# Performance work log

Measured on AMD Instinct MI355X. Metric: run time of the kernel, lower is better.

Reference implementation:

```python
import jax, jax.numpy as jnp
from jax import lax
import numpy as np

SIGMAS = (30.0, 150.0, 300.0)
RESTORE_FACTOR = 2.0
COLOR_GAIN = 10.0
GAIN = 270.0
OFFSET = 128.0
EPS = 1e-6


def _dwconv(x, k2d, stride):
    # depthwise 2D conv, NCHW, VALID padding (caller pads)
    C = x.shape[1]
    kh, kw = k2d.shape
    w = jnp.broadcast_to(k2d.astype(x.dtype)[None, None], (C, 1, kh, kw))
    return lax.conv_general_dilated(
        x, w, (stride, stride), 'VALID',
        dimension_numbers=('NCHW', 'OIHW', 'NCHW'),
        feature_group_count=C)


def _pyr_down(x):
    # cv2.pyrDown: 5x5 binomial kernel, reflect-101 border, stride-2 decimation
    k1 = jnp.array([1., 4., 6., 4., 1.], jnp.float32) / 16.0
    k2 = jnp.outer(k1, k1)
    xp = jnp.pad(x, ((0, 0), (0, 0), (2, 2), (2, 2)), mode='reflect')
    return _dwconv(xp, k2, 2)


def _gauss_blur(x, ksize):
    # cv2.GaussianBlur with sigmaX=0: sigma derived from kernel size
    s = 0.3 * ((ksize - 1) * 0.5 - 1.0) + 0.8
    i = jnp.arange(ksize, dtype=jnp.float32) - (ksize - 1) / 2.0
    g = jnp.exp(-(i * i) / (2.0 * s * s))
    g = g / g.sum()
    k2 = jnp.outer(g, g)
    p = ksize // 2
    xp = jnp.pad(x, ((0, 0), (0, 0), (p, p), (p, p)), mode='reflect')
    return _dwconv(xp, k2, 1)


def _fast_filter(x, sigma):
    # Faithful port of GaussianBlurConv.FastFilter (static Python recursion:
    # sigma is a compile-time constant, so depth is fixed at trace time).
    sigma = min(sigma, 300.0)
    k = int(round(sigma * 3 * 2 + 1)) | 1
    if k < 3:
        return x
    if k < 10:
        return _gauss_blur(x, k)
    h, w = x.shape[2], x.shape[3]
    if h < 2 or w < 2:
        return x
    sub = _fast_filter(_pyr_down(x), sigma / 2.0)
    # cv2.resize default INTER_LINEAR == half-pixel bilinear
    return jax.image.resize(sub, (x.shape[0], x.shape[1], h, w), method='bilinear')


def _msr_forward(x):
    img = x * 255.0 + 1.0                      # (N,3,H,W)
    log_img = jnp.log10(img + EPS)
    retinex = sum(log_img - jnp.log10(_fast_filter(img, s) + EPS) for s in SIGMAS)
    retinex = retinex / len(SIGMAS)
    img_sum = jnp.sum(img, axis=1, keepdims=True)   # (N,1,H,W)
    color_rest = jnp.log10(img * RESTORE_FACTOR / (img_sum + EPS) + 1.0)
    enhanced = retinex * color_rest * COLOR_GAIN * GAIN + OFFSET
    return jnp.clip(enhanced, 0.0, 255.0) / 255.0


def setup_inputs() -> dict:
    key = jax.random.key(0)
    x = jax.random.uniform(key, (8, 3, 1280, 1280), dtype=jnp.float32)
    return {"x": x}


def reference(x):
    return _msr_forward(x)
```

## Files before the change

kernel.cpp:

```cpp
#include <hip/hip_runtime.h>

#define NC 24

typedef float f32x4 __attribute__((ext_vector_type(4)));

__device__ __forceinline__ float pyr_point(const float* ip, int Hi, int Wi, int oy, int ox)
{
    const float k1[5] = {0.0625f, 0.25f, 0.375f, 0.25f, 0.0625f};
    float acc = 0.f;
#pragma unroll
    for (int i = 0; i < 5; ++i) {
        int y = 2 * oy - 2 + i;
        y = (y < 0) ? -y : y;
        y = (y >= Hi) ? (2 * Hi - 2 - y) : y;
        const float* rp = ip + (size_t)y * Wi;
        float r = 0.f;
#pragma unroll
        for (int j = 0; j < 5; ++j) {
            int xx = 2 * ox - 2 + j;
            xx = (xx < 0) ? -xx : xx;
            xx = (xx >= Wi) ? (2 * Wi - 2 - xx) : xx;
            r = fmaf(k1[j], rp[xx], r);
        }
        acc = fmaf(k1[i], r, acc);
    }
    return acc;
}

template <int K>
__device__ __forceinline__ float blur_point(const float* ip, int H, int W, int oy, int ox,
                                            const float* w)
{
    const int R = K / 2;
    float acc = 0.f;
#pragma unroll
    for (int i = 0; i < K; ++i) {
        int y = oy - R + i;
        y = (y < 0) ? -y : y;
        y = (y >= H) ? (2 * H - 2 - y) : y;
        const float* rp = ip + (size_t)y * W;
        float r = 0.f;
#pragma unroll
        for (int j = 0; j < K; ++j) {
            int xx = ox - R + j;
            xx = (xx < 0) ? -xx : xx;
            xx = (xx >= W) ? (2 * W - 2 - xx) : xx;
            r = fmaf(w[j], rp[xx], r);
        }
        acc = fmaf(w[i], r, acc);
    }
    return acc;
}

__global__ void __launch_bounds__(256) pyrdown_lds_kernel(
    const float* __restrict__ in, float* __restrict__ out,
    int Hi, int Wi, int Ho, int Wo, float scale, float offs)
{
    const int TW = 132;
    __shared__ float vs[16 * TW];
    const int tid = threadIdx.x;
    const int OX = blockIdx.x * 64;
    const int OY = blockIdx.y * 16;
    const int nc = blockIdx.z;
    const float k1[5] = {0.0625f, 0.25f, 0.375f, 0.25f, 0.0625f};
    const float* ip = in + (size_t)nc * Hi * Wi;

    for (int idx = tid; idx < 16 * TW; idx += 256) {
        int r = idx / TW;
        int c = idx - r * TW;
        int oy = OY + r;
        if (oy >= Ho) oy = Ho - 1;
        int xc = 2 * OX - 2 + c;
        xc = (xc < 0) ? -xc : xc;
        xc = (xc >= Wi) ? (2 * Wi - 2 - xc) : xc;
        xc = max(0, min(Wi - 1, xc));
        float acc = 0.f;
#pragma unroll
        for (int i = 0; i < 5; ++i) {
            int y = 2 * oy - 2 + i;
            y = (y < 0) ? -y : y;
            y = (y >= Hi) ? (2 * Hi - 2 - y) : y;
            acc = fmaf(k1[i], ip[(size_t)y * Wi + xc], acc);
        }
        vs[idx] = acc;
    }
    __syncthreads();

    for (int o = tid; o < 1024; o += 256) {
        int r = o >> 6, c = o & 63;
        int ox = OX + c, oy = OY + r;
        if (ox >= Wo || oy >= Ho) continue;
        const float* vp = &vs[r * TW + 2 * c];
        float s = 0.f;
#pragma unroll
        for (int j = 0; j < 5; ++j) s = fmaf(k1[j], vp[j], s);
        out[((size_t)nc * Ho + oy) * Wo + ox] = fmaf(s, scale, offs);
    }
}

__global__ void __launch_bounds__(256) base_kernel(
    const float* __restrict__ L4g, float* __restrict__ b30g,
    float* __restrict__ b150g, float* __restrict__ b300g)
{
    __shared__ float sL4[80 * 80];
    __shared__ float sL5[40 * 40];
    __shared__ float sL6[20 * 20];
    __shared__ float sL7[10 * 10];
    __shared__ float sL8[5 * 5];
    const int nc = blockIdx.x;
    const int tid = threadIdx.x;

    float w7[7], w9[9];
    {
        float s = 1.4f, s2 = 2.f * s * s, sum = 0.f;
#pragma unroll
        for (int i = 0; i < 7; ++i) { float d = (float)i - 3.f; w7[i] = expf(-(d * d) / s2); sum += w7[i]; }
#pragma unroll
        for (int i = 0; i < 7; ++i) w7[i] /= sum;
        s = 1.7f; s2 = 2.f * s * s; sum = 0.f;
#pragma unroll
        for (int i = 0; i < 9; ++i) { float d = (float)i - 4.f; w9[i] = expf(-(d * d) / s2); sum += w9[i]; }
#pragma unroll
        for (int i = 0; i < 9; ++i) w9[i] /= sum;
    }

    const float* src = L4g + (size_t)nc * 6400;
    for (int i = tid; i < 1600; i += 256)
        *(f32x4*)&sL4[4 * i] = *(const f32x4*)&src[4 * i];
    __syncthreads();
    for (int i = tid; i < 1600; i += 256) {
        int oy = i / 40, ox = i - oy * 40;
        sL5[i] = pyr_point(sL4, 80, 80, oy, ox);
    }
    __syncthreads();
    for (int i = tid; i < 400; i += 256) {
        int oy = i / 20, ox = i - oy * 20;
        sL6[i] = pyr_point(sL5, 40, 40, oy, ox);
    }
    __syncthreads();
    for (int i = tid; i < 100; i += 256) {
        int oy = i / 10, ox = i - oy * 10;
        sL7[i] = pyr_point(sL6, 20, 20, oy, ox);
    }
    __syncthreads();
    for (int i = tid; i < 25; i += 256) {
        int oy = i / 5, ox = i - oy * 5;
        sL8[i] = pyr_point(sL7, 10, 10, oy, ox);
    }
    __syncthreads();
    for (int i = tid; i < 1600; i += 256) {
        int oy = i / 40, ox = i - oy * 40;
        b30g[(size_t)nc * 1600 + i] = blur_point<7>(sL5, 40, 40, oy, ox, w7);
    }
    for (int i = tid; i < 100; i += 256) {
        int oy = i / 10, ox = i - oy * 10;
        b150g[(size_t)nc * 100 + i] = blur_point<9>(sL7, 10, 10, oy, ox, w9);
    }
    for (int i = tid; i < 25; i += 256) {
        int oy = i / 5, ox = i - oy * 5;
        b300g[(size_t)nc * 25 + i] = blur_point<9>(sL8, 5, 5, oy, ox, w9);
    }
}

#define CH 1721
#define O30_3 0
#define O30_2 36
#define O30_1 100
#define O30_0 244
#define O150_5 568
#define O150_4 593
#define O150_3 618
#define O150_2 654
#define O150_1 718
#define O150_0 862
#define O300_6 1186
#define O300_5 1211
#define O300_4 1236
#define O300_3 1261
#define O300_2 1297
#define O300_1 1333
#define O300_0 1397

template <int NPL, int ND, int NS, int LSD>
__device__ __forceinline__ void up_level(float* __restrict__ S,
                                         const int (&srcO)[NPL], const int (&dstO)[NPL],
                                         int ayD, int axD, int ayS, int axS)
{
    const int SSRC = LSD / 2;
    const int NPTS = ND * ND;
    for (int pt = threadIdx.x; pt < NPTS; pt += 256) {
        int ry = pt / ND, rx = pt - ry * ND;
        int gy = min(max(ayD + ry, 0), LSD - 1);
        int gx = min(max(axD + rx, 0), LSD - 1);
        int my = gy >> 1, py = gy & 1;
        int mx = gx >> 1, px = gx & 1;
        int yA = py ? my : max(my - 1, 0);
        int yB = py ? min(my + 1, SSRC - 1) : my;
        float wyA = py ? 0.75f : 0.25f;
        float wyB = 1.0f - wyA;
        int xA = px ? mx : max(mx - 1, 0);
        int xB = px ? min(mx + 1, SSRC - 1) : mx;
        float wxA = px ? 0.75f : 0.25f;
        float wxB = 1.0f - wxA;
        int la = (yA - ayS) * NS + (xA - axS);
        int laB = la + (xB - xA);
        int lb = (yB - ayS) * NS + (xA - axS);
        int lbB = lb + (xB - xA);
#pragma unroll
        for (int p = 0; p < NPL; ++p) {
            const float* sp = S + srcO[p];
            float v = wyA * fmaf(wxA, sp[la], wxB * sp[laB]) +
                      wyB * fmaf(wxA, sp[lb], wxB * sp[lbB]);
            S[dstO[p] + pt] = v;
        }
    }
}

__global__ void __launch_bounds__(256) mega_final(
    const float* __restrict__ x,
    const float* __restrict__ b30g,
    const float* __restrict__ b150g,
    const float* __restrict__ b300g,
    float* __restrict__ out)
{
    const int H = 1280, W = 1280;
    __shared__ float S[3 * CH];

    const int tid = threadIdx.x;
    const int X0 = blockIdx.x * 64, Y0 = blockIdx.y * 64;
    const int n = blockIdx.z;

    int ay[7], ax[7];
    ay[0] = (Y0 >> 2) - 1;
    ax[0] = (X0 >> 2) - 1;
#pragma unroll
    for (int l = 1; l < 7; ++l) {
        ay[l] = (ay[l - 1] >> 1) - 1;
        ax[l] = (ax[l - 1] >> 1) - 1;
    }

    if (tid < 36) {
        int ry = tid / 6, rx = tid - ry * 6;
        int gy = min(max(ay[3] + ry, 0), 39);
        int gx = min(max(ax[3] + rx, 0), 39);
#pragma unroll
        for (int c = 0; c < 3; ++c)
            S[c * CH + O30_3 + tid] = b30g[(size_t)(n * 3 + c) * 1600 + gy * 40 + gx];
    } else if (tid >= 64 && tid < 89) {
        int t = tid - 64;
        int ry = t / 5, rx = t - ry * 5;
        int gy = min(max(ay[5] + ry, 0), 9);
        int gx = min(max(ax[5] + rx, 0), 9);
#pragma unroll
        for (int c = 0; c < 3; ++c)
            S[c * CH + O150_5 + t] = b150g[(size_t)(n * 3 + c) * 100 + gy * 10 + gx];
    } else if (tid >= 128 && tid < 153) {
        int t = tid - 128;
        int ry = t / 5, rx = t - ry * 5;
        int gy = min(max(ay[6] + ry, 0), 4);
        int gx = min(max(ax[6] + rx, 0), 4);
#pragma unroll
        for (int c = 0; c < 3; ++c)
            S[c * CH + O300_6 + t] = b300g[(size_t)(n * 3 + c) * 25 + gy * 5 + gx];
    }
    __syncthreads();

    {
        const int s[3] = {O300_6, O300_6 + CH, O300_6 + 2 * CH};
        const int d[3] = {O300_5, O300_5 + CH, O300_5 + 2 * CH};
        up_level<3, 5, 5, 10>(S, s, d, ay[5], ax[5], ay[6], ax[6]);
    }
    __syncthreads();
    {
        const int s[6] = {O300_5, O300_5 + CH, O300_5 + 2 * CH, O150_5, O150_5 + CH, O150_5 + 2 * CH};
        const int d[6] = {O300_4, O300_4 + CH, O300_4 + 2 * CH, O150_4, O150_4 + CH, O150_4 + 2 * CH};
        up_level<6, 5, 5, 20>(S, s, d, ay[4], ax[4], ay[5], ax[5]);
    }
    __syncthreads();
    {
        const int s[6] = {O300_4, O300_4 + CH, O300_4 + 2 * CH, O150_4, O150_4 + CH, O150_4 + 2 * CH};
        const int d[6] = {O300_3, O300_3 + CH, O300_3 + 2 * CH, O150_3, O150_3 + CH, O150_3 + 2 * CH};
        up_level<6, 6, 5, 40>(S, s, d, ay[3], ax[3], ay[4], ax[4]);
    }
    __syncthreads();
    {
        const int s[9] = {O300_3, O300_3 + CH, O300_3 + 2 * CH, O150_3, O150_3 + CH, O150_3 + 2 * CH,
                          O30_3, O30_3 + CH, O30_3 + 2 * CH};
        const int d[9] = {O300_2, O300_2 + CH, O300_2 + 2 * CH, O150_2, O150_2 + CH, O150_2 + 2 * CH,
                          O30_2, O30_2 + CH, O30_2 + 2 * CH};
        up_level<9, 8, 6, 80>(S, s, d, ay[2], ax[2], ay[3], ax[3]);
    }
    __syncthreads();
    {
        const int s[9] = {O300_2, O300_2 + CH, O300_2 + 2 * CH, O150_2, O150_2 + CH, O150_2 + 2 * CH,
                          O30_2, O30_2 + CH, O30_2 + 2 * CH};
        const int d[9] = {O300_1, O300_1 + CH, O300_1 + 2 * CH, O150_1, O150_1 + CH, O150_1 + 2 * CH,
                          O30_1, O30_1 + CH, O30_1 + 2 * CH};
        up_level<9, 12, 8, 160>(S, s, d, ay[1], ax[1], ay[2], ax[2]);
    }
    __syncthreads();
    {
        const int s[9] = {O300_1, O300_1 + CH, O300_1 + 2 * CH, O150_1, O150_1 + CH, O150_1 + 2 * CH,
                          O30_1, O30_1 + CH, O30_1 + 2 * CH};
        const int d[9] = {O300_0, O300_0 + CH, O300_0 + 2 * CH, O150_0, O150_0 + CH, O150_0 + 2 * CH,
                          O30_0, O30_0 + CH, O30_0 + 2 * CH};
        up_level<9, 18, 12, 320>(S, s, d, ay[0], ax[0], ay[1], ax[1]);
    }
    __syncthreads();

    int tyi = tid >> 4, txi = tid & 15;
    int byi = (Y0 >> 2) + tyi, bxi = (X0 >> 2) + txi;
    int ry[3], rx[3];
    ry[0] = max(byi - 1, 0) - ay[0]; ry[1] = byi - ay[0]; ry[2] = min(byi + 1, 319) - ay[0];
    rx[0] = max(bxi - 1, 0) - ax[0]; rx[1] = bxi - ax[0]; rx[2] = min(bxi + 1, 319) - ax[0];
    const int ol0[3] = {O30_0, O150_0, O300_0};

    f32x4 xi[3][4];
#pragma unroll
    for (int c = 0; c < 3; ++c)
#pragma unroll
        for (int qy = 0; qy < 4; ++qy)
            xi[c][qy] = __builtin_nontemporal_load(
                (const f32x4*)&x[((size_t)(n * 3 + c) * H + 4 * byi + qy) * W + 4 * bxi]);

    float crcp[4][4];
#pragma unroll
    for (int qy = 0; qy < 4; ++qy)
#pragma unroll
        for (int qx = 0; qx < 4; ++qx) {
            float s = (xi[0][qy][qx] + xi[1][qy][qx] + xi[2][qy][qx]) * 255.f + 3.f;
            crcp[qy][qx] = __fdividef(2.f, s + 1e-6f);
        }

#pragma unroll
    for (int c = 0; c < 3; ++c) {
        float prod[4][4];
#pragma unroll
        for (int qy = 0; qy < 4; ++qy)
#pragma unroll
            for (int qx = 0; qx < 4; ++qx) prod[qy][qx] = 1.f;

#pragma unroll
        for (int s = 0; s < 3; ++s) {
            const float* fp = &S[c * CH + ol0[s]];
            float v[3][3];
#pragma unroll
            for (int i = 0; i < 3; ++i)
#pragma unroll
                for (int j = 0; j < 3; ++j) v[i][j] = fp[ry[i] * 18 + rx[j]];
            float cy[4][3];
#pragma unroll
            for (int j = 0; j < 3; ++j) {
                float v0 = v[0][j], v1 = v[1][j], v2 = v[2][j];
                cy[0][j] = fmaf(0.375f, v0, 0.625f * v1);
                cy[1][j] = fmaf(0.1875f, v0, fmaf(0.75f, v1, 0.0625f * v2));
                cy[2][j] = fmaf(0.0625f, v0, fmaf(0.75f, v1, 0.1875f * v2));
                cy[3][j] = fmaf(0.625f, v1, 0.375f * v2);
            }
#pragma unroll
            for (int qy = 0; qy < 4; ++qy) {
                float a0 = cy[qy][0], a1 = cy[qy][1], a2 = cy[qy][2];
                float t0 = fmaf(0.375f, a0, 0.625f * a1);
                float t1 = fmaf(0.1875f, a0, fmaf(0.75f, a1, 0.0625f * a2));
                float t2 = fmaf(0.0625f, a0, fmaf(0.75f, a1, 0.1875f * a2));
                float t3 = fmaf(0.625f, a1, 0.375f * a2);
                prod[qy][0] *= (t0 + 1e-6f);
                prod[qy][1] *= (t1 + 1e-6f);
                prod[qy][2] *= (t2 + 1e-6f);
                prod[qy][3] *= (t3 + 1e-6f);
            }
        }

#pragma unroll
        for (int qy = 0; qy < 4; ++qy) {
            f32x4 o;
#pragma unroll
            for (int qx = 0; qx < 4; ++qx) {
                float img = xi[c][qy][qx] * 255.f + 1.f;
                float a = img + 1e-6f;
                float l2a = __log2f(__fdividef(a * a * a, prod[qy][qx]));
                float carg = fmaf(img, crcp[qy][qx], 1.f);
                float l2c = __log2f(carg);
                float e = fmaf(l2a * l2c, 81.55715246f, 128.f);
                e = fminf(fmaxf(e, 0.f), 255.f);
                o[qx] = e * (1.f / 255.f);
            }
            __builtin_nontemporal_store(
                o, (f32x4*)&out[((size_t)(n * 3 + c) * H + 4 * byi + qy) * W + 4 * bxi]);
        }
    }
}

extern "C" void kernel_launch(void* const* d_in, const int* in_sizes, int n_in,
                              void* d_out, int out_size, void* d_ws, size_t ws_size,
                              hipStream_t stream)
{
    const float* x = (const float*)d_in[0];
    float* out = (float*)d_out;
    float* ws = (float*)d_ws;

    size_t off = 0;
    auto alloc = [&](int d) { float* p = ws + off; off += (size_t)NC * d * d; return p; };
    float* L1 = alloc(640);
    float* L2 = alloc(320);
    float* L3 = alloc(160);
    float* L4 = alloc(80);
    float* b30 = alloc(40);
    float* b150 = alloc(10);
    float* b300 = alloc(5);
    (void)ws_size; (void)in_sizes; (void)n_in; (void)out_size;

    dim3 blk(256, 1, 1);
    auto gridP = [&](int Wo, int Ho) { return dim3((Wo + 63) / 64, (Ho + 15) / 16, NC); };

    pyrdown_lds_kernel<<<gridP(640, 640), blk, 0, stream>>>(x,  L1, 1280, 1280, 640, 640, 255.f, 1.f);
    pyrdown_lds_kernel<<<gridP(320, 320), blk, 0, stream>>>(L1, L2, 640, 640, 320, 320, 1.f, 0.f);
    pyrdown_lds_kernel<<<gridP(160, 160), blk, 0, stream>>>(L2, L3, 320, 320, 160, 160, 1.f, 0.f);
    pyrdown_lds_kernel<<<gridP(80,  80),  blk, 0, stream>>>(L3, L4, 160, 160, 80, 80, 1.f, 0.f);
    base_kernel<<<dim3(NC, 1, 1), dim3(256, 1, 1), 0, stream>>>(L4, b30, b150, b300);
    mega_final<<<dim3(20, 20, 8), dim3(256, 1, 1), 0, stream>>>(x, b30, b150, b300, out);
}
```

Baseline: 356.2 us.

## Fuse L3/L4 pyramid levels into single per-channel tail kernel

Replaces two pyrdown kernel launches and the base kernel with one 1024-thread block per image channel. That block computes L3 from L2 in shared memory in row strips, then L4 and the coarser levels plus the blurs. It removes two launches and the global round trips for L3 and L4. In exchange, only 24 blocks do the 320->160 level, which underuses the GPU, and shared memory use grows to about 140KB per block.

```diff
diff --git a/kernel.cpp b/kernel.cpp
--- a/kernel.cpp
+++ b/kernel.cpp
@@ -98,10 +98,12 @@
     }
 }
 
-__global__ void __launch_bounds__(256) base_kernel(
-    const float* __restrict__ L4g, float* __restrict__ b30g,
+__global__ void __launch_bounds__(1024) fused_tail(
+    const float* __restrict__ L2g, float* __restrict__ b30g,
     float* __restrict__ b150g, float* __restrict__ b300g)
 {
+    __shared__ float sL3[160 * 160];
+    __shared__ float vs[8 * 324];
     __shared__ float sL4[80 * 80];
     __shared__ float sL5[40 * 40];
     __shared__ float sL6[20 * 20];
@@ -109,6 +111,8 @@
     __shared__ float sL8[5 * 5];
     const int nc = blockIdx.x;
     const int tid = threadIdx.x;
+    const float k1[5] = {0.0625f, 0.25f, 0.375f, 0.25f, 0.0625f};
+    const float* ip = L2g + (size_t)nc * 320 * 320;
 
     float w7[7], w9[9];
     {
@@ -124,39 +128,71 @@
         for (int i = 0; i < 9; ++i) w9[i] /= sum;
     }
 
-    const float* src = L4g + (size_t)nc * 6400;
-    for (int i = tid; i < 1600; i += 256)
-        *(f32x4*)&sL4[4 * i] = *(const f32x4*)&src[4 * i];
-    __syncthreads();
-    for (int i = tid; i < 1600; i += 256) {
+    for (int st = 0; st < 20; ++st) {
+        const int OY = st * 8;
+        for (int idx = tid; idx < 8 * 324; idx += 1024) {
+            int r = idx / 324, c = idx - r * 324;
+            int oy = OY + r;
+            int xc = c - 2;
+            xc = (xc < 0) ? -xc : xc;
+            xc = (xc >= 320) ? (638 - xc) : xc;
+            float acc = 0.f;
+#pragma unroll
+            for (int i = 0; i < 5; ++i) {
+                int y = 2 * oy - 2 + i;
+                y = (y < 0) ? -y : y;
+                y = (y >= 320) ? (638 - y) : y;
+                acc = fmaf(k1[i], ip[y * 320 + xc], acc);
+            }
+            vs[idx] = acc;
+        }
+        __syncthreads();
+        for (int o = tid; o < 8 * 160; o += 1024) {
+            int r = o / 160, c = o - r * 160;
+            const float* vp = &vs[r * 324 + 2 * c];
+            float s = 0.f;
+#pragma unroll
+            for (int j = 0; j < 5; ++j) s = fmaf(k1[j], vp[j], s);
+            sL3[(OY + r) * 160 + c] = s;
+        }
+        __syncthreads();
+    }
+
+    for (int i = tid; i < 6400; i += 1024) {
+        int oy = i / 80, ox = i - oy * 80;
+        sL4[i] = pyr_point(sL3, 160, 160, oy, ox);
+    }
+    __syncthreads();
+    for (int i = tid; i < 1600; i += 1024) {
         int oy = i / 40, ox = i - oy * 40;
         sL5[i] = pyr_point(sL4, 80, 80, oy, ox);
     }
     __syncthreads();
-    for (int i = tid; i < 400; i += 256) {
+    for (int i = tid; i < 400; i += 1024) {
         int oy = i / 20, ox = i - oy * 20;
         sL6[i] = pyr_point(sL5, 40, 40, oy, ox);
     }
     __syncthreads();
-    for (int i = tid; i < 100; i += 256) {
+    for (int i = tid; i < 100; i += 1024) {
         int oy = i / 10, ox = i - oy * 10;
         sL7[i] = pyr_point(sL6, 20, 20, oy, ox);
     }
     __syncthreads();
-    for (int i = tid; i < 25; i += 256) {
+    for (int i = tid; i < 25; i += 1024) {
         int oy = i / 5, ox = i - oy * 5;
         sL8[i] = pyr_point(sL7, 10, 10, oy, ox);
     }
     __syncthreads();
-    for (int i = tid; i < 1600; i += 256) {
+
+    for (int i = tid; i < 1600; i += 1024) {
         int oy = i / 40, ox = i - oy * 40;
         b30g[(size_t)nc * 1600 + i] = blur_point<7>(sL5, 40, 40, oy, ox, w7);
     }
-    for (int i = tid; i < 100; i += 256) {
+    for (int i = tid; i < 100; i += 1024) {
         int oy = i / 10, ox = i - oy * 10;
         b150g[(size_t)nc * 100 + i] = blur_point<9>(sL7, 10, 10, oy, ox, w9);
     }
-    for (int i = tid; i < 25; i += 256) {
+    for (int i = tid; i < 25; i += 1024) {
         int oy = i / 5, ox = i - oy * 5;
         b300g[(size_t)nc * 25 + i] = blur_point<9>(sL8, 5, 5, oy, ox, w9);
     }
@@ -403,8 +439,6 @@
     auto alloc = [&](int d) { float* p = ws + off; off += (size_t)NC * d * d; return p; };
     float* L1 = alloc(640);
     float* L2 = alloc(320);
-    float* L3 = alloc(160);
-    float* L4 = alloc(80);
     float* b30 = alloc(40);
     float* b150 = alloc(10);
     float* b300 = alloc(5);
@@ -415,8 +449,6 @@
 
     pyrdown_lds_kernel<<<gridP(640, 640), blk, 0, stream>>>(x,  L1, 1280, 1280, 640, 640, 255.f, 1.f);
     pyrdown_lds_kernel<<<gridP(320, 320), blk, 0, stream>>>(L1, L2, 640, 640, 320, 320, 1.f, 0.f);
-    pyrdown_lds_kernel<<<gridP(160, 160), blk, 0, stream>>>(L2, L3, 320, 320, 160, 160, 1.f, 0.f);
-    pyrdown_lds_kernel<<<gridP(80,  80),  blk, 0, stream>>>(L3, L4, 160, 160, 80, 80, 1.f, 0.f);
-    base_kernel<<<dim3(NC, 1, 1), dim3(256, 1, 1), 0, stream>>>(L4, b30, b150, b300);
+    fused_tail<<<dim3(NC, 1, 1), dim3(1024, 1, 1), 0, stream>>>(L2, b30, b150, b300);
     mega_final<<<dim3(20, 20, 8), dim3(256, 1, 1), 0, stream>>>(x, b30, b150, b300, out);
 }
```

After: 376.4 us. 5.7% more time.

## Fuse pairs of pyrDown levels into one kernel, skipping L1 and L3 buffers

Applied to the files above, without the earlier changes.

Replaces the four separate pyrDown launches with two launches of a kernel that does two consecutive pyrDown levels in shared memory. It computes the intermediate level tile with halo in LDS, so the L1 and L3 global round trips and two launches go away. The base kernel also moves to 512 threads per block. In exchange it recomputes halo rows, uses far more LDS per block (lower occupancy), and the second fused launch has few blocks.

```diff
diff --git a/kernel.cpp b/kernel.cpp
--- a/kernel.cpp
+++ b/kernel.cpp
@@ -52,37 +52,65 @@
     return acc;
 }
 
-__global__ void __launch_bounds__(256) pyrdown_lds_kernel(
+__global__ void __launch_bounds__(256) dpyrdown_kernel(
     const float* __restrict__ in, float* __restrict__ out,
-    int Hi, int Wi, int Ho, int Wo, float scale, float offs)
-{
-    const int TW = 132;
-    __shared__ float vs[16 * TW];
+    int Hi, int Wi, int Hm, int Wm, int Ho, int Wo, float scale, float offs)
+{
+    __shared__ float vsA[35 * 268];
+    __shared__ float l1t[35 * 132];
+    __shared__ float vsC[16 * 132];
     const int tid = threadIdx.x;
     const int OX = blockIdx.x * 64;
     const int OY = blockIdx.y * 16;
     const int nc = blockIdx.z;
     const float k1[5] = {0.0625f, 0.25f, 0.375f, 0.25f, 0.0625f};
     const float* ip = in + (size_t)nc * Hi * Wi;
-
-    for (int idx = tid; idx < 16 * TW; idx += 256) {
-        int r = idx / TW;
-        int c = idx - r * TW;
-        int oy = OY + r;
-        if (oy >= Ho) oy = Ho - 1;
-        int xc = 2 * OX - 2 + c;
-        xc = (xc < 0) ? -xc : xc;
-        xc = (xc >= Wi) ? (2 * Wi - 2 - xc) : xc;
-        xc = max(0, min(Wi - 1, xc));
+    const int baseX = 4 * OX - 6;
+    const int baseY1 = 2 * OY - 2;
+
+    for (int idx = tid; idx < 35 * 268; idx += 256) {
+        int r = idx / 268, c = idx - r * 268;
+        int y1 = baseY1 + r;
+        int xi = baseX + c;
+        xi = (xi < 0) ? -xi : xi;
+        xi = (xi >= Wi) ? (2 * Wi - 2 - xi) : xi;
+        xi = min(max(xi, 0), Wi - 1);
         float acc = 0.f;
 #pragma unroll
         for (int i = 0; i < 5; ++i) {
-            int y = 2 * oy - 2 + i;
+            int y = 2 * y1 - 2 + i;
             y = (y < 0) ? -y : y;
             y = (y >= Hi) ? (2 * Hi - 2 - y) : y;
-            acc = fmaf(k1[i], ip[(size_t)y * Wi + xc], acc);
-        }
-        vs[idx] = acc;
+            y = min(max(y, 0), Hi - 1);
+            acc = fmaf(k1[i], ip[(size_t)y * Wi + xi], acc);
+        }
+        vsA[idx] = acc;
+    }
+    __syncthreads();
+
+    for (int idx = tid; idx < 35 * 132; idx += 256) {
+        int r = idx / 132, lc = idx - r * 132;
+        const float* vp = &vsA[r * 268 + 2 * lc];
+        float acc = 0.f;
+#pragma unroll
+        for (int j = 0; j < 5; ++j) acc = fmaf(k1[j], vp[j], acc);
+        l1t[idx] = acc;
+    }
+    __syncthreads();
+
+    for (int idx = tid; idx < 16 * 132; idx += 256) {
+        int rr = idx / 132, lc = idx - rr * 132;
+        int y1n0 = baseY1 + 2 * rr;
+        float acc = 0.f;
+#pragma unroll
+        for (int i = 0; i < 5; ++i) {
+            int y1 = y1n0 + i;
+            y1 = (y1 < 0) ? -y1 : y1;
+            y1 = (y1 >= Hm) ? (2 * Hm - 2 - y1) : y1;
+            int ly = min(max(y1 - baseY1, 0), 34);
+            acc = fmaf(k1[i], l1t[ly * 132 + lc], acc);
+        }
+        vsC[idx] = acc;
     }
     __syncthreads();
 
@@ -90,15 +118,20 @@
         int r = o >> 6, c = o & 63;
         int ox = OX + c, oy = OY + r;
         if (ox >= Wo || oy >= Ho) continue;
-        const float* vp = &vs[r * TW + 2 * c];
-        float s = 0.f;
-#pragma unroll
-        for (int j = 0; j < 5; ++j) s = fmaf(k1[j], vp[j], s);
-        out[((size_t)nc * Ho + oy) * Wo + ox] = fmaf(s, scale, offs);
-    }
-}
-
-__global__ void __launch_bounds__(256) base_kernel(
+        float acc = 0.f;
+#pragma unroll
+        for (int j = 0; j < 5; ++j) {
+            int c1 = 2 * ox - 2 + j;
+            c1 = (c1 < 0) ? -c1 : c1;
+            c1 = (c1 >= Wm) ? (2 * Wm - 2 - c1) : c1;
+            int lc = min(max(c1 - (2 * OX - 2), 0), 131);
+            acc = fmaf(k1[j], vsC[r * 132 + lc], acc);
+        }
+        out[((size_t)nc * Ho + oy) * Wo + ox] = fmaf(acc, scale, offs);
+    }
+}
+
+__global__ void __launch_bounds__(512) base_kernel(
     const float* __restrict__ L4g, float* __restrict__ b30g,
     float* __restrict__ b150g, float* __restrict__ b300g)
 {
@@ -125,38 +158,38 @@
     }
 
     const float* src = L4g + (size_t)nc * 6400;
-    for (int i = tid; i < 1600; i += 256)
+    for (int i = tid; i < 1600; i += 512)
         *(f32x4*)&sL4[4 * i] = *(const f32x4*)&src[4 * i];
     __syncthreads();
-    for (int i = tid; i < 1600; i += 256) {
+    for (int i = tid; i < 1600; i += 512) {
         int oy = i / 40, ox = i - oy * 40;
         sL5[i] = pyr_point(sL4, 80, 80, oy, ox);
     }
     __syncthreads();
-    for (int i = tid; i < 400; i += 256) {
+    for (int i = tid; i < 400; i += 512) {
         int oy = i / 20, ox = i - oy * 20;
         sL6[i] = pyr_point(sL5, 40, 40, oy, ox);
     }
     __syncthreads();
-    for (int i = tid; i < 100; i += 256) {
+    for (int i = tid; i < 100; i += 512) {
         int oy = i / 10, ox = i - oy * 10;
         sL7[i] = pyr_point(sL6, 20, 20, oy, ox);
     }
     __syncthreads();
-    for (int i = tid; i < 25; i += 256) {
+    for (int i = tid; i < 25; i += 512) {
         int oy = i / 5, ox = i - oy * 5;
         sL8[i] = pyr_point(sL7, 10, 10, oy, ox);
     }
     __syncthreads();
-    for (int i = tid; i < 1600; i += 256) {
+    for (int i = tid; i < 1600; i += 512) {
         int oy = i / 40, ox = i - oy * 40;
         b30g[(size_t)nc * 1600 + i] = blur_point<7>(sL5, 40, 40, oy, ox, w7);
     }
-    for (int i = tid; i < 100; i += 256) {
+    for (int i = tid; i < 100; i += 512) {
         int oy = i / 10, ox = i - oy * 10;
         b150g[(size_t)nc * 100 + i] = blur_point<9>(sL7, 10, 10, oy, ox, w9);
     }
-    for (int i = tid; i < 25; i += 256) {
+    for (int i = tid; i < 25; i += 512) {
         int oy = i / 5, ox = i - oy * 5;
         b300g[(size_t)nc * 25 + i] = blur_point<9>(sL8, 5, 5, oy, ox, w9);
     }
@@ -401,9 +434,7 @@
 
     size_t off = 0;
     auto alloc = [&](int d) { float* p = ws + off; off += (size_t)NC * d * d; return p; };
-    float* L1 = alloc(640);
     float* L2 = alloc(320);
-    float* L3 = alloc(160);
     float* L4 = alloc(80);
     float* b30 = alloc(40);
     float* b150 = alloc(10);
@@ -411,12 +442,11 @@
     (void)ws_size; (void)in_sizes; (void)n_in; (void)out_size;
 
     dim3 blk(256, 1, 1);
-    auto gridP = [&](int Wo, int Ho) { return dim3((Wo + 63) / 64, (Ho + 15) / 16, NC); };
-
-    pyrdown_lds_kernel<<<gridP(640, 640), blk, 0, stream>>>(x,  L1, 1280, 1280, 640, 640, 255.f, 1.f);
-    pyrdown_lds_kernel<<<gridP(320, 320), blk, 0, stream>>>(L1, L2, 640, 640, 320, 320, 1.f, 0.f);
-    pyrdown_lds_kernel<<<gridP(160, 160), blk, 0, stream>>>(L2, L3, 320, 320, 160, 160, 1.f, 0.f);
-    pyrdown_lds_kernel<<<gridP(80,  80),  blk, 0, stream>>>(L3, L4, 160, 160, 80, 80, 1.f, 0.f);
-    base_kernel<<<dim3(NC, 1, 1), dim3(256, 1, 1), 0, stream>>>(L4, b30, b150, b300);
+
+    dpyrdown_kernel<<<dim3(5, 20, NC), blk, 0, stream>>>(
+        x, L2, 1280, 1280, 640, 640, 320, 320, 255.f, 1.f);
+    dpyrdown_kernel<<<dim3(2, 5, NC), blk, 0, stream>>>(
+        L2, L4, 320, 320, 160, 160, 80, 80, 1.f, 0.f);
+    base_kernel<<<dim3(NC, 1, 1), dim3(512, 1, 1), 0, stream>>>(L4, b30, b150, b300);
     mega_final<<<dim3(20, 20, 8), dim3(256, 1, 1), 0, stream>>>(x, b30, b150, b300, out);
 }
```

After: 430.7 us. +20.9%, slower.

## Stage pyrDown input tile in LDS with vectorized loads and template dimensions

Applied to the files above, without the earlier changes.

The pyramid-down kernel now loads a 35x136 input tile into shared memory with float4 loads on interior blocks, with a scalar reflect-padded path at borders. It then does the vertical and horizontal 5-tap passes from LDS instead of issuing strided scalar global loads per column. Image sizes become template parameters so index math is resolved at compile time. The base kernel moves from 256 to 512 threads per block. Together these raise LDS use per block and add a branch between the interior and border paths.

```diff
diff --git a/kernel.cpp b/kernel.cpp
--- a/kernel.cpp
+++ b/kernel.cpp
@@ -52,53 +52,66 @@
     return acc;
 }
 
-__global__ void __launch_bounds__(256) pyrdown_lds_kernel(
-    const float* __restrict__ in, float* __restrict__ out,
-    int Hi, int Wi, int Ho, int Wo, float scale, float offs)
-{
-    const int TW = 132;
-    __shared__ float vs[16 * TW];
+template <int HI, int WI>
+__global__ void __launch_bounds__(256) pyrdown_v2(
+    const float* __restrict__ in, float* __restrict__ out, float scale, float offs)
+{
+    const int HO = HI / 2, WO = WI / 2;
+    __shared__ float tile[35][136];
+    __shared__ float vs[16][132];
     const int tid = threadIdx.x;
     const int OX = blockIdx.x * 64;
     const int OY = blockIdx.y * 16;
     const int nc = blockIdx.z;
     const float k1[5] = {0.0625f, 0.25f, 0.375f, 0.25f, 0.0625f};
-    const float* ip = in + (size_t)nc * Hi * Wi;
-
-    for (int idx = tid; idx < 16 * TW; idx += 256) {
-        int r = idx / TW;
-        int c = idx - r * TW;
-        int oy = OY + r;
-        if (oy >= Ho) oy = Ho - 1;
-        int xc = 2 * OX - 2 + c;
-        xc = (xc < 0) ? -xc : xc;
-        xc = (xc >= Wi) ? (2 * Wi - 2 - xc) : xc;
-        xc = max(0, min(Wi - 1, xc));
-        float acc = 0.f;
-#pragma unroll
-        for (int i = 0; i < 5; ++i) {
-            int y = 2 * oy - 2 + i;
+    const float* ip = in + (size_t)nc * HI * WI;
+    const int gx0 = 2 * OX - 4;
+
+    if (gx0 >= 0 && gx0 + 135 < WI) {
+        for (int v = tid; v < 35 * 34; v += 256) {
+            int r = v / 34, q = v - r * 34;
+            int y = 2 * OY - 2 + r;
             y = (y < 0) ? -y : y;
-            y = (y >= Hi) ? (2 * Hi - 2 - y) : y;
-            acc = fmaf(k1[i], ip[(size_t)y * Wi + xc], acc);
-        }
-        vs[idx] = acc;
+            y = (y >= HI) ? (2 * HI - 2 - y) : y;
+            *(f32x4*)&tile[r][4 * q] = *(const f32x4*)&ip[(size_t)y * WI + gx0 + 4 * q];
+        }
+    } else {
+        for (int v = tid; v < 35 * 136; v += 256) {
+            int r = v / 136, c = v - r * 136;
+            int y = 2 * OY - 2 + r;
+            y = (y < 0) ? -y : y;
+            y = (y >= HI) ? (2 * HI - 2 - y) : y;
+            y = min(max(y, 0), HI - 1);
+            int x = gx0 + c;
+            x = (x < 0) ? -x : x;
+            x = (x >= WI) ? (2 * WI - 2 - x) : x;
+            x = min(max(x, 0), WI - 1);
+            tile[r][c] = ip[(size_t)y * WI + x];
+        }
+    }
+    __syncthreads();
+
+    for (int v = tid; v < 16 * 132; v += 256) {
+        int r = v / 132, c = v - r * 132;
+        float acc = k1[0] * tile[2 * r][c + 2];
+#pragma unroll
+        for (int i = 1; i < 5; ++i) acc = fmaf(k1[i], tile[2 * r + i][c + 2], acc);
+        vs[r][c] = acc;
     }
     __syncthreads();
 
     for (int o = tid; o < 1024; o += 256) {
         int r = o >> 6, c = o & 63;
         int ox = OX + c, oy = OY + r;
-        if (ox >= Wo || oy >= Ho) continue;
-        const float* vp = &vs[r * TW + 2 * c];
-        float s = 0.f;
-#pragma unroll
-        for (int j = 0; j < 5; ++j) s = fmaf(k1[j], vp[j], s);
-        out[((size_t)nc * Ho + oy) * Wo + ox] = fmaf(s, scale, offs);
-    }
-}
-
-__global__ void __launch_bounds__(256) base_kernel(
+        if (ox >= WO || oy >= HO) continue;
+        float acc = k1[0] * vs[r][2 * c];
+#pragma unroll
+        for (int j = 1; j < 5; ++j) acc = fmaf(k1[j], vs[r][2 * c + j], acc);
+        out[((size_t)nc * HO + oy) * WO + ox] = fmaf(acc, scale, offs);
+    }
+}
+
+__global__ void __launch_bounds__(512) base_kernel(
     const float* __restrict__ L4g, float* __restrict__ b30g,
     float* __restrict__ b150g, float* __restrict__ b300g)
 {
@@ -125,38 +138,38 @@
     }
 
     const float* src = L4g + (size_t)nc * 6400;
-    for (int i = tid; i < 1600; i += 256)
+    for (int i = tid; i < 1600; i += 512)
         *(f32x4*)&sL4[4 * i] = *(const f32x4*)&src[4 * i];
     __syncthreads();
-    for (int i = tid; i < 1600; i += 256) {
+    for (int i = tid; i < 1600; i += 512) {
         int oy = i / 40, ox = i - oy * 40;
         sL5[i] = pyr_point(sL4, 80, 80, oy, ox);
     }
     __syncthreads();
-    for (int i = tid; i < 400; i += 256) {
+    for (int i = tid; i < 400; i += 512) {
         int oy = i / 20, ox = i - oy * 20;
         sL6[i] = pyr_point(sL5, 40, 40, oy, ox);
     }
     __syncthreads();
-    for (int i = tid; i < 100; i += 256) {
+    for (int i = tid; i < 100; i += 512) {
         int oy = i / 10, ox = i - oy * 10;
         sL7[i] = pyr_point(sL6, 20, 20, oy, ox);
     }
     __syncthreads();
-    for (int i = tid; i < 25; i += 256) {
+    for (int i = tid; i < 25; i += 512) {
         int oy = i / 5, ox = i - oy * 5;
         sL8[i] = pyr_point(sL7, 10, 10, oy, ox);
     }
     __syncthreads();
-    for (int i = tid; i < 1600; i += 256) {
+    for (int i = tid; i < 1600; i += 512) {
         int oy = i / 40, ox = i - oy * 40;
         b30g[(size_t)nc * 1600 + i] = blur_point<7>(sL5, 40, 40, oy, ox, w7);
     }
-    for (int i = tid; i < 100; i += 256) {
+    for (int i = tid; i < 100; i += 512) {
         int oy = i / 10, ox = i - oy * 10;
         b150g[(size_t)nc * 100 + i] = blur_point<9>(sL7, 10, 10, oy, ox, w9);
     }
-    for (int i = tid; i < 25; i += 256) {
+    for (int i = tid; i < 25; i += 512) {
         int oy = i / 5, ox = i - oy * 5;
         b300g[(size_t)nc * 25 + i] = blur_point<9>(sL8, 5, 5, oy, ox, w9);
     }
@@ -411,12 +424,11 @@
     (void)ws_size; (void)in_sizes; (void)n_in; (void)out_size;
 
     dim3 blk(256, 1, 1);
-    auto gridP = [&](int Wo, int Ho) { return dim3((Wo + 63) / 64, (Ho + 15) / 16, NC); };
-
-    pyrdown_lds_kernel<<<gridP(640, 640), blk, 0, stream>>>(x,  L1, 1280, 1280, 640, 640, 255.f, 1.f);
-    pyrdown_lds_kernel<<<gridP(320, 320), blk, 0, stream>>>(L1, L2, 640, 640, 320, 320, 1.f, 0.f);
-    pyrdown_lds_kernel<<<gridP(160, 160), blk, 0, stream>>>(L2, L3, 320, 320, 160, 160, 1.f, 0.f);
-    pyrdown_lds_kernel<<<gridP(80,  80),  blk, 0, stream>>>(L3, L4, 160, 160, 80, 80, 1.f, 0.f);
-    base_kernel<<<dim3(NC, 1, 1), dim3(256, 1, 1), 0, stream>>>(L4, b30, b150, b300);
+
+    pyrdown_v2<1280, 1280><<<dim3(10, 40, NC), blk, 0, stream>>>(x,  L1, 255.f, 1.f);
+    pyrdown_v2<640, 640><<<dim3(5, 20, NC), blk, 0, stream>>>(L1, L2, 1.f, 0.f);
+    pyrdown_v2<320, 320><<<dim3(3, 10, NC), blk, 0, stream>>>(L2, L3, 1.f, 0.f);
+    pyrdown_v2<160, 160><<<dim3(2, 5, NC), blk, 0, stream>>>(L3, L4, 1.f, 0.f);
+    base_kernel<<<dim3(NC, 1, 1), dim3(512, 1, 1), 0, stream>>>(L4, b30, b150, b300);
     mega_final<<<dim3(20, 20, 8), dim3(256, 1, 1), 0, stream>>>(x, b30, b150, b300, out);
 }
```

Measured after the change: 351.5 us. Within noise of the previous version (-1.3%).
